# Optimization experiments

Measured on AMD Instinct MI355X. Metric: run time of the kernel, lower is better.

## Reference

```python
import jax, jax.numpy as jnp
import numpy as np

D = 512      # word_embedding_dim (dim_in == dim_out)
HEADS = 8    # isab_num_heads
M = 16       # isab_num_inds
B = 2048     # batch_news_num = batch_size * news_num
S = 32       # max_title_length
EPS = 1e-5   # torch LayerNorm default eps


def _layer_norm(x, g, b):
    mu = jnp.mean(x, axis=-1, keepdims=True)
    var = jnp.mean((x - mu) ** 2, axis=-1, keepdims=True)
    return (x - mu) * jax.lax.rsqrt(var + EPS) * g + b


def _mab(Qin, Kin, Wqkv, bqkv, Wo, bo, g0, b0, g1, b1):
    # Faithful to torch MAB: linear Q/K/V, head split via reshape (equivalent
    # to split/cat since cat-back restores head slices), scale by sqrt(dim_V).
    d = Wqkv.shape[-1]
    Q = Qin @ Wqkv[0] + bqkv[0]          # [B, Sq, d]
    K = Kin @ Wqkv[1] + bqkv[1]          # [B, Sk, d]
    V = Kin @ Wqkv[2] + bqkv[2]
    Bn, Sq, _ = Q.shape
    Sk = K.shape[1]
    hd = d // HEADS
    Qh = Q.reshape(Bn, Sq, HEADS, hd)
    Kh = K.reshape(Bn, Sk, HEADS, hd)
    Vh = V.reshape(Bn, Sk, HEADS, hd)
    scores = jnp.einsum('bqhd,bkhd->bhqk', Qh, Kh) / jnp.sqrt(jnp.asarray(d, Q.dtype))
    A = jax.nn.softmax(scores, axis=-1)
    Oh = Qh + jnp.einsum('bhqk,bkhd->bqhd', A, Vh)   # residual on Q_
    O = Oh.reshape(Bn, Sq, d)
    O = _layer_norm(O, g0, b0)                        # ln0
    O = O + jax.nn.relu(O @ Wo + bo)                  # O + relu(fc_o(O))
    O = _layer_norm(O, g1, b1)                        # ln1
    return O


def _isab(X, I, p0, p1):
    Iq = jnp.broadcast_to(I, (X.shape[0],) + I.shape[1:])  # I.repeat(B,1,1)
    Hm = _mab(Iq, X, *p0)   # mab0(I, X) -> [B, M, d]
    return _mab(X, Hm, *p1)  # mab1(X, H) -> [B, S, d]


def setup_inputs() -> dict:
    key = jax.random.key(0)
    ks = jax.random.split(key, 12)
    sc = 1.0 / np.sqrt(D)
    inp = {
        'x': jax.random.normal(ks[0], (B, S, D), dtype=jnp.float32),
        'I': jax.random.normal(ks[1], (1, M, D), dtype=jnp.float32) * sc,
        'mab0_Wqkv': jax.random.normal(ks[2], (3, D, D), dtype=jnp.float32) * sc,
        'mab0_bqkv': jnp.zeros((3, D), dtype=jnp.float32),
        'mab0_Wo': jax.random.normal(ks[3], (D, D), dtype=jnp.float32) * sc,
        'mab0_bo': jnp.zeros((D,), dtype=jnp.float32),
        'mab0_g0': jnp.ones((D,), dtype=jnp.float32),
        'mab0_b0': jnp.zeros((D,), dtype=jnp.float32),
        'mab0_g1': jnp.ones((D,), dtype=jnp.float32),
        'mab0_b1': jnp.zeros((D,), dtype=jnp.float32),
        'mab1_Wqkv': jax.random.normal(ks[4], (3, D, D), dtype=jnp.float32) * sc,
        'mab1_bqkv': jnp.zeros((3, D), dtype=jnp.float32),
        'mab1_Wo': jax.random.normal(ks[5], (D, D), dtype=jnp.float32) * sc,
        'mab1_bo': jnp.zeros((D,), dtype=jnp.float32),
        'mab1_g0': jnp.ones((D,), dtype=jnp.float32),
        'mab1_b0': jnp.zeros((D,), dtype=jnp.float32),
        'mab1_g1': jnp.ones((D,), dtype=jnp.float32),
        'mab1_b1': jnp.zeros((D,), dtype=jnp.float32),
    }
    return inp


def reference(x, I,
              mab0_Wqkv, mab0_bqkv, mab0_Wo, mab0_bo, mab0_g0, mab0_b0, mab0_g1, mab0_b1,
              mab1_Wqkv, mab1_bqkv, mab1_Wo, mab1_bo, mab1_g0, mab1_b0, mab1_g1, mab1_b1):
    p0 = (mab0_Wqkv, mab0_bqkv, mab0_Wo, mab0_bo, mab0_g0, mab0_b0, mab0_g1, mab0_b1)
    p1 = (mab1_Wqkv, mab1_bqkv, mab1_Wo, mab1_bo, mab1_g0, mab1_b0, mab1_g1, mab1_b1)
    # CIDER title path (eval mode, dropout=identity): ISAB applied twice, mean pool
    h1 = _isab(x, I, p0, p1)
    h2 = _isab(h1, I, p0, p1)
    return jnp.mean(h2, axis=1)   # [B, D] title_embedding
```

## Files before the change

### kernel.cpp

```cpp
#include <hip/hip_runtime.h>
#include <hip/hip_bf16.h>

#define D 512
#define BATCH 2048
#define SEQ 32
#define MIND 16

typedef __hip_bfloat16 bf16;
typedef __attribute__((ext_vector_type(8))) short s8v;
typedef __attribute__((ext_vector_type(4))) short s4v;
typedef __attribute__((ext_vector_type(4))) float f4v;

#define SWZ(row, kb) (((row) << 10) + ((kb) ^ (((row) & 7) << 4)))

__device__ __forceinline__ ushort f2bu(float f) {
    bf16 h = __float2bfloat16(f); ushort u; __builtin_memcpy(&u, &h, 2); return u;
}
__device__ __forceinline__ float bu2f(ushort u) {
    unsigned x = ((unsigned)u) << 16; float f; __builtin_memcpy(&f, &x, 4); return f;
}

__device__ __forceinline__ float wave_sum(float v) {
#pragma unroll
    for (int off = 32; off >= 1; off >>= 1) v += __shfl_xor(v, off, 64);
    return v;
}

struct WPtrs { const float* s[7]; };

__global__ __launch_bounds__(256) void wtrans7(WPtrs wp, ushort* __restrict__ Wt) {
    const float* W = wp.s[blockIdx.z];
    ushort* dst = Wt + (size_t)blockIdx.z * 262144;
    __shared__ float t[32][33];
    const int k0 = blockIdx.x * 32, n0 = blockIdx.y * 32;
    const int lx = threadIdx.x & 31, ly = threadIdx.x >> 5;
    for (int i = ly; i < 32; i += 8) t[i][lx] = W[(size_t)(k0 + i) * D + n0 + lx];
    __syncthreads();
    for (int i = ly; i < 32; i += 8)
        dst[(size_t)(n0 + i) * D + k0 + lx] = f2bu(t[lx][i]);
}

__global__ __launch_bounds__(256) void q0_kernel(
    const float* __restrict__ I, const float* __restrict__ Wq,
    const float* __restrict__ bq, ushort* __restrict__ Q0b)
{
    const int q = blockIdx.x;
    const int c = threadIdx.x;
    float a0 = 0.f, a1 = 0.f;
    for (int k = 0; k < D; ++k) {
        const float iv = I[q * D + k];
        a0 = fmaf(iv, Wq[(size_t)k * D + c], a0);
        a1 = fmaf(iv, Wq[(size_t)k * D + c + 256], a1);
    }
    Q0b[q * D + c]       = f2bu(a0 + bq[c]);
    Q0b[q * D + c + 256] = f2bu(a1 + bq[c + 256]);
}

__global__ __launch_bounds__(256) void conv_bf16(const float* __restrict__ x,
                                                 ushort* __restrict__ xb, long n4) {
    for (long i = (long)blockIdx.x * 256 + threadIdx.x; i < n4; i += (long)gridDim.x * 256) {
        const float4 v = ((const float4*)x)[i];
        s4v o = {(short)f2bu(v.x), (short)f2bu(v.y), (short)f2bu(v.z), (short)f2bu(v.w)};
        ((s4v*)xb)[i] = o;
    }
}

template <int NOUT, bool RESFUSE, bool LNA, bool SPARSEA>
__global__ __launch_bounds__(512, 4) void gemmN(
    const ushort* __restrict__ Ab,
    const ushort* __restrict__ Wt0, const float* __restrict__ bias0, ushort* __restrict__ C0,
    const ushort* __restrict__ Wt1, const float* __restrict__ bias1, ushort* __restrict__ C1,
    const ushort* __restrict__ Wt2, const float* __restrict__ bias2, ushort* __restrict__ C2,
    const float* __restrict__ lng, const float* __restrict__ lnb)
{
    __shared__ __align__(16) char sA[64 * 1024];
    __shared__ __align__(16) char sC[16 * 1024];
    const int tid = threadIdx.x, lane = tid & 63, wv = tid >> 6;
    const size_t m0 = (size_t)blockIdx.x * 64;

    for (int c = tid; c < 64 * 64; c += 512) {
        const int row = c >> 6, k8 = (c & 63) << 3;
        const size_t L = m0 + row;
        const size_t pr = SPARSEA ? ((L >> 4) * 32 + (L & 15)) : L;
        *(s8v*)(sA + SWZ(row, k8 * 2)) = *(const s8v*)(Ab + pr * D + k8);
    }
    __syncthreads();

    if constexpr (LNA) {
        for (int i = wv; i < 64; i += 8) {
            float v[8];
#pragma unroll
            for (int j = 0; j < 8; ++j)
                v[j] = bu2f(*(const ushort*)(sA + SWZ(i, 2 * (lane + 64 * j))));
            float s = 0.f;
#pragma unroll
            for (int j = 0; j < 8; ++j) s += v[j];
            s = wave_sum(s);
            const float mu = s * (1.f / 512.f);
            float q2 = 0.f;
#pragma unroll
            for (int j = 0; j < 8; ++j) { const float t = v[j] - mu; q2 = fmaf(t, t, q2); }
            q2 = wave_sum(q2);
            const float inv = rsqrtf(q2 * (1.f / 512.f) + 1e-5f);
#pragma unroll
            for (int j = 0; j < 8; ++j) {
                const int d0 = lane + 64 * j;
                *(ushort*)(sA + SWZ(i, 2 * d0)) = f2bu((v[j] - mu) * inv * lng[d0] + lnb[d0]);
            }
        }
        __syncthreads();
    }

    const int m = lane & 15, g = lane >> 4;
    const int swm = (m & 7) << 4;
    const ushort* Wts[3]  = {Wt0, Wt1, Wt2};
    const float*  bias[3] = {bias0, bias1, bias2};
    ushort*       Cs[3]   = {C0, C1, C2};

#pragma unroll
    for (int o = 0; o < NOUT; ++o) {
        const ushort* Bp = Wts[o] + ((size_t)(wv * 64 + m) << 9) + 8 * g;
        f4v acc[4][4];
#pragma unroll
        for (int i = 0; i < 4; ++i)
#pragma unroll
            for (int j = 0; j < 4; ++j) acc[i][j] = (f4v){0.f, 0.f, 0.f, 0.f};

#pragma unroll
        for (int k0 = 0; k0 < 512; k0 += 32) {
            s8v bfr[4];
#pragma unroll
            for (int ct = 0; ct < 4; ++ct) bfr[ct] = *(const s8v*)(Bp + ct * 8192 + k0);
            const int kb = 2 * (k0 + 8 * g);
            s8v a[4];
#pragma unroll
            for (int rt = 0; rt < 4; ++rt)
                a[rt] = *(const s8v*)(sA + ((rt * 16 + m) << 10) + (kb ^ swm));
#pragma unroll
            for (int ct = 0; ct < 4; ++ct)
#pragma unroll
                for (int rt = 0; rt < 4; ++rt)
                    acc[rt][ct] = __builtin_amdgcn_mfma_f32_16x16x32_bf16(a[rt], bfr[ct], acc[rt][ct], 0, 0, 0);
        }

        ushort* Cb = Cs[o];
        const float* bb = bias[o];
#pragma unroll
        for (int rt = 0; rt < 4; ++rt) {
            __syncthreads();
#pragma unroll
            for (int ct = 0; ct < 4; ++ct) {
                const int col = wv * 64 + ct * 16 + m;
                const float bv = bb[col];
#pragma unroll
                for (int r = 0; r < 4; ++r) {
                    const int lrow = g * 4 + r;
                    float v = acc[rt][ct][r] + bv;
                    if (RESFUSE)
                        v = bu2f(*(const ushort*)(sA + SWZ(rt * 16 + lrow, 2 * col))) + fmaxf(v, 0.f);
                    *(ushort*)(sC + SWZ(lrow, 2 * col)) = f2bu(v);
                }
            }
            __syncthreads();
            for (int c = tid; c < 16 * 64; c += 512) {
                const int row = c >> 6, k8 = (c & 63) << 3;
                *(s8v*)(Cb + (m0 + rt * 16 + row) * D + k8) = *(const s8v*)(sC + SWZ(row, k8 * 2));
            }
        }
        __syncthreads();
    }
}

template <int SQ, int SK, bool QSHARED, int OSTR>
__global__ __launch_bounds__(64) void attn_core(
    const ushort* __restrict__ Qb, const ushort* __restrict__ Kb,
    const ushort* __restrict__ Vb, ushort* __restrict__ Ob)
{
    constexpr int RS = 72;
    __shared__ __align__(16) ushort sQ[SQ * RS];
    __shared__ __align__(16) ushort sK[SK * RS];
    __shared__ __align__(16) ushort sV[SK * RS];
    __shared__ float sS[SQ][SK + 1];

    const int lane = threadIdx.x;
    const int b = blockIdx.x, h = blockIdx.y;
    const size_t qbase = (QSHARED ? (size_t)0 : (size_t)b * SQ * D) + h * 64;
    const size_t kbase = (size_t)b * SK * D + h * 64;

    for (int idx = lane; idx < SQ * 16; idx += 64) {
        const int r = idx >> 4, c4 = (idx & 15) << 2;
        *(s4v*)(sQ + r * RS + c4) = *(const s4v*)(Qb + qbase + (size_t)r * D + c4);
    }
    for (int idx = lane; idx < SK * 16; idx += 64) {
        const int r = idx >> 4, c4 = (idx & 15) << 2;
        *(s4v*)(sK + r * RS + c4) = *(const s4v*)(Kb + kbase + (size_t)r * D + c4);
        *(s4v*)(sV + r * RS + c4) = *(const s4v*)(Vb + kbase + (size_t)r * D + c4);
    }
    __syncthreads();

    const float scale = 0.044194173824159216f;
#pragma unroll
    for (int o = 0; o < SQ * SK / 64; ++o) {
        const int idx = o * 64 + lane;
        const int q = idx / SK, k = idx % SK;
        float s = 0.f;
#pragma unroll
        for (int dd = 0; dd < 64; dd += 8) {
            const s8v aq = *(const s8v*)(sQ + q * RS + dd);
            const s8v ak = *(const s8v*)(sK + k * RS + dd);
#pragma unroll
            for (int e = 0; e < 8; ++e)
                s = fmaf(bu2f((ushort)aq[e]), bu2f((ushort)ak[e]), s);
        }
        sS[q][k] = s * scale;
    }
    __syncthreads();

    if (lane < SQ) {
        float* row = sS[lane];
        float mx = row[0];
#pragma unroll
        for (int k = 1; k < SK; ++k) mx = fmaxf(mx, row[k]);
        float sum = 0.f;
#pragma unroll
        for (int k = 0; k < SK; ++k) { const float e = __expf(row[k] - mx); row[k] = e; sum += e; }
        const float inv = 1.f / sum;
#pragma unroll
        for (int k = 0; k < SK; ++k) row[k] *= inv;
    }
    __syncthreads();

    float acc[SQ];
#pragma unroll
    for (int q = 0; q < SQ; ++q) acc[q] = 0.f;
#pragma unroll 4
    for (int k = 0; k < SK; ++k) {
        const float v = bu2f(sV[k * RS + lane]);
#pragma unroll
        for (int q = 0; q < SQ; ++q) acc[q] = fmaf(sS[q][k], v, acc[q]);
    }
    const size_t obase = (size_t)b * OSTR * D + h * 64 + lane;
#pragma unroll
    for (int q = 0; q < SQ; ++q)
        Ob[obase + (size_t)q * D] = f2bu(bu2f(sQ[q * RS + lane]) + acc[q]);
}

__global__ __launch_bounds__(512) void ln_meanpool(
    const ushort* __restrict__ U, const float* __restrict__ gg,
    const float* __restrict__ bb, float* __restrict__ outp)
{
    __shared__ float sP[8][512];
    const int tid = threadIdx.x, lane = tid & 63, wv = tid >> 6;
    const size_t b = blockIdx.x;
    float a[8];
#pragma unroll
    for (int j = 0; j < 8; ++j) a[j] = 0.f;
    for (int i = wv; i < 32; i += 8) {
        const ushort* u = U + ((size_t)b * 32 + i) * D;
        float v[8];
#pragma unroll
        for (int j = 0; j < 8; ++j) v[j] = bu2f(u[lane + 64 * j]);
        float s = 0.f;
#pragma unroll
        for (int j = 0; j < 8; ++j) s += v[j];
        s = wave_sum(s);
        const float mu = s * (1.f / 512.f);
        float q2 = 0.f;
#pragma unroll
        for (int j = 0; j < 8; ++j) { const float t = v[j] - mu; q2 = fmaf(t, t, q2); }
        q2 = wave_sum(q2);
        const float inv = rsqrtf(q2 * (1.f / 512.f) + 1e-5f);
#pragma unroll
        for (int j = 0; j < 8; ++j) {
            const int d0 = lane + 64 * j;
            a[j] += (v[j] - mu) * inv * gg[d0] + bb[d0];
        }
    }
#pragma unroll
    for (int j = 0; j < 8; ++j) sP[wv][lane + 64 * j] = a[j];
    __syncthreads();
    float s = 0.f;
#pragma unroll
    for (int w = 0; w < 8; ++w) s += sP[w][tid];
    outp[b * D + tid] = s * (1.f / 32.f);
}

extern "C" void kernel_launch(void* const* d_in, const int* in_sizes, int n_in,
                              void* d_out, int out_size, void* d_ws, size_t ws_size,
                              hipStream_t stream) {
    (void)in_sizes; (void)n_in; (void)out_size; (void)ws_size;

    const float* x     = (const float*)d_in[0];
    const float* I     = (const float*)d_in[1];
    const float* W0    = (const float*)d_in[2];
    const float* bqkv0 = (const float*)d_in[3];
    const float* Wo0   = (const float*)d_in[4];
    const float* bo0   = (const float*)d_in[5];
    const float* g00   = (const float*)d_in[6];
    const float* b00   = (const float*)d_in[7];
    const float* g01   = (const float*)d_in[8];
    const float* b01   = (const float*)d_in[9];
    const float* W1    = (const float*)d_in[10];
    const float* bqkv1 = (const float*)d_in[11];
    const float* Wo1   = (const float*)d_in[12];
    const float* bo1   = (const float*)d_in[13];
    const float* g10   = (const float*)d_in[14];
    const float* b10   = (const float*)d_in[15];
    const float* g11   = (const float*)d_in[16];
    const float* b11   = (const float*)d_in[17];

    const float* Wq0 = W0;     const float* Wk0 = W0 + D * D;  const float* Wv0 = W0 + 2 * D * D;
    const float* bq0 = bqkv0;  const float* bk0 = bqkv0 + D;   const float* bv0 = bqkv0 + 2 * D;
    const float* Wq1 = W1;     const float* Wk1 = W1 + D * D;  const float* Wv1 = W1 + 2 * D * D;
    const float* bq1 = bqkv1;  const float* bk1 = bqkv1 + D;   const float* bv1 = bqkv1 + 2 * D;

    char* ws = (char*)d_ws;
    ushort* Q0b = (ushort*)ws;
    ushort* Wt  = (ushort*)(ws + 32768);
    char* base = ws + 32768 + 7 * 524288;
    ushort* P0 = (ushort*)(base);
    ushort* P1 = (ushort*)(base + ((size_t)64 << 20));
    ushort* P2 = (ushort*)(base + ((size_t)128 << 20));
    ushort* P3 = (ushort*)(base + ((size_t)192 << 20));
    const size_t HALFE = (size_t)16 << 20;
    ushort* P1hi = P1 + HALFE;

    ushort* WtK0 = Wt + 0 * 262144;
    ushort* WtV0 = Wt + 1 * 262144;
    ushort* WtO0 = Wt + 2 * 262144;
    ushort* WtQ1 = Wt + 3 * 262144;
    ushort* WtK1 = Wt + 4 * 262144;
    ushort* WtV1 = Wt + 5 * 262144;
    ushort* WtO1 = Wt + 6 * 262144;

    WPtrs wp; wp.s[0] = Wk0; wp.s[1] = Wv0; wp.s[2] = Wo0; wp.s[3] = Wq1;
    wp.s[4] = Wk1; wp.s[5] = Wv1; wp.s[6] = Wo1;
    wtrans7<<<dim3(16, 16, 7), 256, 0, stream>>>(wp, Wt);
    q0_kernel<<<MIND, 256, 0, stream>>>(I, Wq0, bq0, Q0b);
    conv_bf16<<<4096, 256, 0, stream>>>(x, P0, (long)BATCH * SEQ * D / 4);

    constexpr int GBS = BATCH * SEQ / 64;
    constexpr int GBM = BATCH * MIND / 64;
    const dim3 ag(BATCH, 8);

    for (int isab = 0; isab < 2; ++isab) {
        if (isab == 0)
            gemmN<3, false, false, false><<<GBS, 512, 0, stream>>>(
                P0, WtK0, bk0, P1, WtV0, bv0, P2, WtQ1, bq1, P3, nullptr, nullptr);
        else
            gemmN<3, false, true, false><<<GBS, 512, 0, stream>>>(
                P0, WtK0, bk0, P1, WtV0, bv0, P2, WtQ1, bq1, P3, g11, b11);
        attn_core<MIND, SEQ, true, 32><<<ag, 64, 0, stream>>>(Q0b, P1, P2, P1);
        gemmN<1, true, true, true><<<GBM, 512, 0, stream>>>(
            P1, WtO0, bo0, P2, nullptr, nullptr, nullptr, nullptr, nullptr, nullptr, g00, b00);
        gemmN<2, false, true, false><<<GBM, 512, 0, stream>>>(
            P2, WtK1, bk1, P1, WtV1, bv1, P1hi, nullptr, nullptr, nullptr, g01, b01);
        attn_core<SEQ, MIND, false, 32><<<ag, 64, 0, stream>>>(P3, P1, P1hi, P3);
        gemmN<1, true, true, false><<<GBS, 512, 0, stream>>>(
            P3, WtO1, bo1, P0, nullptr, nullptr, nullptr, nullptr, nullptr, nullptr, g10, b10);
    }

    ln_meanpool<<<BATCH, 512, 0, stream>>>(P0, g11, b11, (float*)d_out);
}
```

Before: 1.481 ms.

## Fuse fp32-to-bf16 input conversion into first GEMM, prefetch B fragments, nontemporal I/O

Drops the separate conv_bf16 pass. The first QKV GEMM now reads fp32 x directly and converts it to bf16 while staging into shared memory, which removes one full write and read of the activation tensor. The GEMM inner loop also double-buffers the weight fragments by loading the next k-step while the MFMAs run, and activation loads and output stores use nontemporal hints. These add register pressure (bnxt buffers) under launch bounds of 4 blocks per CU, and the nontemporal stores may hurt reuse by the next kernel, which reads these outputs right away.

New measurement: 1.373 ms. 1.08x faster.

```diff
diff --git a/kernel.cpp b/kernel.cpp
--- a/kernel.cpp
+++ b/kernel.cpp
@@ -56,18 +56,9 @@
     Q0b[q * D + c + 256] = f2bu(a1 + bq[c + 256]);
 }
 
-__global__ __launch_bounds__(256) void conv_bf16(const float* __restrict__ x,
-                                                 ushort* __restrict__ xb, long n4) {
-    for (long i = (long)blockIdx.x * 256 + threadIdx.x; i < n4; i += (long)gridDim.x * 256) {
-        const float4 v = ((const float4*)x)[i];
-        s4v o = {(short)f2bu(v.x), (short)f2bu(v.y), (short)f2bu(v.z), (short)f2bu(v.w)};
-        ((s4v*)xb)[i] = o;
-    }
-}
-
-template <int NOUT, bool RESFUSE, bool LNA, bool SPARSEA>
+template <int NOUT, bool RESFUSE, bool LNA, bool SPARSEA, bool AF32>
 __global__ __launch_bounds__(512, 4) void gemmN(
-    const ushort* __restrict__ Ab,
+    const ushort* __restrict__ Ab, const float* __restrict__ Af,
     const ushort* __restrict__ Wt0, const float* __restrict__ bias0, ushort* __restrict__ C0,
     const ushort* __restrict__ Wt1, const float* __restrict__ bias1, ushort* __restrict__ C1,
     const ushort* __restrict__ Wt2, const float* __restrict__ bias2, ushort* __restrict__ C2,
@@ -82,7 +73,17 @@
         const int row = c >> 6, k8 = (c & 63) << 3;
         const size_t L = m0 + row;
         const size_t pr = SPARSEA ? ((L >> 4) * 32 + (L & 15)) : L;
-        *(s8v*)(sA + SWZ(row, k8 * 2)) = *(const s8v*)(Ab + pr * D + k8);
+        s8v o;
+        if constexpr (AF32) {
+            const float* src = Af + pr * D + k8;
+            const f4v v0 = __builtin_nontemporal_load((const f4v*)src);
+            const f4v v1 = __builtin_nontemporal_load((const f4v*)(src + 4));
+            o = s8v{(short)f2bu(v0.x), (short)f2bu(v0.y), (short)f2bu(v0.z), (short)f2bu(v0.w),
+                    (short)f2bu(v1.x), (short)f2bu(v1.y), (short)f2bu(v1.z), (short)f2bu(v1.w)};
+        } else {
+            o = __builtin_nontemporal_load((const s8v*)(Ab + pr * D + k8));
+        }
+        *(s8v*)(sA + SWZ(row, k8 * 2)) = o;
     }
     __syncthreads();
 
@@ -126,11 +127,15 @@
 #pragma unroll
             for (int j = 0; j < 4; ++j) acc[i][j] = (f4v){0.f, 0.f, 0.f, 0.f};
 
+        s8v bcur[4], bnxt[4];
+#pragma unroll
+        for (int ct = 0; ct < 4; ++ct) bcur[ct] = *(const s8v*)(Bp + ct * 8192);
 #pragma unroll
         for (int k0 = 0; k0 < 512; k0 += 32) {
-            s8v bfr[4];
-#pragma unroll
-            for (int ct = 0; ct < 4; ++ct) bfr[ct] = *(const s8v*)(Bp + ct * 8192 + k0);
+            if (k0 < 480) {
+#pragma unroll
+                for (int ct = 0; ct < 4; ++ct) bnxt[ct] = *(const s8v*)(Bp + ct * 8192 + k0 + 32);
+            }
             const int kb = 2 * (k0 + 8 * g);
             s8v a[4];
 #pragma unroll
@@ -140,7 +145,9 @@
             for (int ct = 0; ct < 4; ++ct)
 #pragma unroll
                 for (int rt = 0; rt < 4; ++rt)
-                    acc[rt][ct] = __builtin_amdgcn_mfma_f32_16x16x32_bf16(a[rt], bfr[ct], acc[rt][ct], 0, 0, 0);
+                    acc[rt][ct] = __builtin_amdgcn_mfma_f32_16x16x32_bf16(a[rt], bcur[ct], acc[rt][ct], 0, 0, 0);
+#pragma unroll
+            for (int ct = 0; ct < 4; ++ct) bcur[ct] = bnxt[ct];
         }
 
         ushort* Cb = Cs[o];
@@ -164,7 +171,8 @@
             __syncthreads();
             for (int c = tid; c < 16 * 64; c += 512) {
                 const int row = c >> 6, k8 = (c & 63) << 3;
-                *(s8v*)(Cb + (m0 + rt * 16 + row) * D + k8) = *(const s8v*)(sC + SWZ(row, k8 * 2));
+                __builtin_nontemporal_store(*(const s8v*)(sC + SWZ(row, k8 * 2)),
+                                            (s8v*)(Cb + (m0 + rt * 16 + row) * D + k8));
             }
         }
         __syncthreads();
@@ -337,7 +345,6 @@
     wp.s[4] = Wk1; wp.s[5] = Wv1; wp.s[6] = Wo1;
     wtrans7<<<dim3(16, 16, 7), 256, 0, stream>>>(wp, Wt);
     q0_kernel<<<MIND, 256, 0, stream>>>(I, Wq0, bq0, Q0b);
-    conv_bf16<<<4096, 256, 0, stream>>>(x, P0, (long)BATCH * SEQ * D / 4);
 
     constexpr int GBS = BATCH * SEQ / 64;
     constexpr int GBM = BATCH * MIND / 64;
@@ -345,19 +352,19 @@
 
     for (int isab = 0; isab < 2; ++isab) {
         if (isab == 0)
-            gemmN<3, false, false, false><<<GBS, 512, 0, stream>>>(
-                P0, WtK0, bk0, P1, WtV0, bv0, P2, WtQ1, bq1, P3, nullptr, nullptr);
+            gemmN<3, false, false, false, true><<<GBS, 512, 0, stream>>>(
+                nullptr, x, WtK0, bk0, P1, WtV0, bv0, P2, WtQ1, bq1, P3, nullptr, nullptr);
         else
-            gemmN<3, false, true, false><<<GBS, 512, 0, stream>>>(
-                P0, WtK0, bk0, P1, WtV0, bv0, P2, WtQ1, bq1, P3, g11, b11);
+            gemmN<3, false, true, false, false><<<GBS, 512, 0, stream>>>(
+                P0, nullptr, WtK0, bk0, P1, WtV0, bv0, P2, WtQ1, bq1, P3, g11, b11);
         attn_core<MIND, SEQ, true, 32><<<ag, 64, 0, stream>>>(Q0b, P1, P2, P1);
-        gemmN<1, true, true, true><<<GBM, 512, 0, stream>>>(
-            P1, WtO0, bo0, P2, nullptr, nullptr, nullptr, nullptr, nullptr, nullptr, g00, b00);
-        gemmN<2, false, true, false><<<GBM, 512, 0, stream>>>(
-            P2, WtK1, bk1, P1, WtV1, bv1, P1hi, nullptr, nullptr, nullptr, g01, b01);
+        gemmN<1, true, true, true, false><<<GBM, 512, 0, stream>>>(
+            P1, nullptr, WtO0, bo0, P2, nullptr, nullptr, nullptr, nullptr, nullptr, nullptr, g00, b00);
+        gemmN<2, false, true, false, false><<<GBM, 512, 0, stream>>>(
+            P2, nullptr, WtK1, bk1, P1, WtV1, bv1, P1hi, nullptr, nullptr, nullptr, g01, b01);
         attn_core<SEQ, MIND, false, 32><<<ag, 64, 0, stream>>>(P3, P1, P1hi, P3);
-        gemmN<1, true, true, false><<<GBS, 512, 0, stream>>>(
-            P3, WtO1, bo1, P0, nullptr, nullptr, nullptr, nullptr, nullptr, nullptr, g10, b10);
+        gemmN<1, true, true, false, false><<<GBS, 512, 0, stream>>>(
+            P3, nullptr, WtO1, bo1, P0, nullptr, nullptr, nullptr, nullptr, nullptr, nullptr, g10, b10);
     }
 
     ln_meanpool<<<BATCH, 512, 0, stream>>>(P0, g11, b11, (float*)d_out);
```
